# Performance work log

Hardware: AMD Instinct MI355X
Metric: run time of the kernel (lower is better)

Reference implementation:

```python
import jax, jax.numpy as jnp
import numpy as np

R = 59        # num relations (58 + 1)
D = 128       # node_feat_size
K = 16        # neighbors_sample


def _lstm(windows, Wk, Wr, b):
    # windows: [N, T, F]; standard Keras LSTM (gate order i, f, g, o).
    N = windows.shape[0]
    z_in = jnp.einsum('ntf,fh->nth', windows, Wk) + b        # [N, T, 4D]
    z_in = jnp.swapaxes(z_in, 0, 1)                          # [T, N, 4D]

    def step(carry, zt):
        h, c = carry
        z = zt + h @ Wr
        i, f, g, o = jnp.split(z, 4, axis=-1)
        i = jax.nn.sigmoid(i)
        f = jax.nn.sigmoid(f)
        g = jnp.tanh(g)
        o = jax.nn.sigmoid(o)
        c = f * c + i * g
        h = o * jnp.tanh(c)
        return (h, c), None

    h0 = jnp.zeros((N, D), windows.dtype)
    (h, _), _ = jax.lax.scan(step, (h0, h0), z_in)
    return h                                                 # [N, D]


def setup_inputs() -> dict:
    key = jax.random.key(0)
    ks = jax.random.split(key, 12)
    N, T, F = 1024, 32, 10
    s = 0.05
    return {
        'windows': jax.random.normal(ks[0], (N, T, F), jnp.float32),
        'neighbors': jax.random.randint(ks[1], (R, N, K), 0, N + 1, jnp.int32),
        'lstm_kernel': jax.random.normal(ks[2], (F, 4 * D), jnp.float32) * s,
        'lstm_recurrent': jax.random.normal(ks[3], (D, 4 * D), jnp.float32) * s,
        'lstm_bias': jax.random.normal(ks[4], (4 * D,), jnp.float32) * s,
        'W_state': jax.random.normal(ks[5], (R, 2 * D + R), jnp.float32) * s,
        'b_state': jax.random.normal(ks[6], (R,), jnp.float32) * s,
        'W_relattn': jax.random.normal(ks[7], (2 * D + R,), jnp.float32) * s,
        'b_relattn': jax.random.normal(ks[8], (1,), jnp.float32) * s,
        'W_pred': jax.random.normal(ks[9], (D, 3), jnp.float32) * s,
        'b_pred': jax.random.normal(ks[10], (3,), jnp.float32) * s,
    }


def reference(windows, neighbors, lstm_kernel, lstm_recurrent, lstm_bias,
              W_state, b_state, W_relattn, b_relattn, W_pred, b_pred):
    cur = _lstm(windows, lstm_kernel, lstm_recurrent, lstm_bias)    # [N, D]
    feats = jnp.concatenate([jnp.zeros((1, D), cur.dtype), cur], 0)  # [N+1, D]

    # --- per-relation state attention ---
    # Dense(1) on concat(cur, nbr, onehot(rel)) splits into three dot products.
    Wc = W_state[:, :D]            # [R, D]
    Wn = W_state[:, D:2 * D]       # [R, D]
    Wrr = W_state[:, 2 * D:]       # [R, R]; onehot picks the diagonal
    rel_term = jnp.diagonal(Wrr) + b_state                  # [R]
    cur_term = cur @ Wc.T                                    # [N, R]
    nbr_proj = feats @ Wn.T                                  # [N+1, R]
    # gather the scalar neighbor projection per relation: [R, N, K]
    nbr_term = jax.vmap(lambda idx, p: p[idx])(neighbors, nbr_proj.T)
    scores = jax.nn.relu(cur_term.T[:, :, None] + nbr_term
                         + rel_term[:, None, None])          # [R, N, K]
    w = jax.nn.softmax(scores, axis=-1)
    nbr_feats = feats[neighbors]                             # [R, N, K, D]
    rel_reps = jnp.einsum('rnk,rnkd->rnd', w, nbr_feats)     # [R, N, D]

    # --- relation attention ---
    wc = W_relattn[:D]
    wn = W_relattn[D:2 * D]
    wr = W_relattn[2 * D:]                                   # [R]
    s2 = jax.nn.relu((cur @ wc)[None, :]
                     + jnp.einsum('rnd,d->rn', rel_reps, wn)
                     + wr[:, None] + b_relattn[0])           # [R, N]
    aw = jax.nn.softmax(s2, axis=0)
    rel_agg = jnp.einsum('rn,rnd->nd', aw, rel_reps)         # [N, D]
    updated = cur + rel_agg

    logits = updated @ W_pred + b_pred                       # [N, 3]
    predictions = jax.nn.softmax(logits, axis=-1)
    return logits, predictions, updated
```

## Files before the change

kernel.cpp:

```cpp
#include <hip/hip_runtime.h>
#include <hip/hip_bf16.h>

constexpr int R  = 59;
constexpr int D  = 128;
constexpr int NK = 16;
constexpr int N  = 1024;
constexpr int T  = 32;
constexpr int F  = 10;
constexpr int H4 = 512;
constexpr int WSTRIDE = 2*D + R;

typedef __attribute__((ext_vector_type(8))) short short8;
typedef __attribute__((ext_vector_type(4))) float f32x4;

__device__ __forceinline__ float sigm(float x) {
  return __builtin_amdgcn_rcpf(1.0f + __expf(-x));
}
__device__ __forceinline__ float tanh_(float x) {
  return 2.0f * __builtin_amdgcn_rcpf(1.0f + __expf(-2.0f * x)) - 1.0f;
}
__device__ __forceinline__ ushort f2bf(float f) {
  unsigned u = __float_as_uint(f);
  u += 0x7FFF + ((u >> 16) & 1);
  return (ushort)(u >> 16);
}

__device__ int g_detect_f32(const void* windows) {
  const __hip_bfloat16* p = (const __hip_bfloat16*)windows;
  int weird = 0;
  for (int i = 0; i < 128; ++i) {
    float v = __bfloat162float(p[i]);
    float a = fabsf(v);
    if (!(a <= 100.0f) || (v != 0.0f && a < 1e-8f)) ++weird;
  }
  return weird > 8;
}

__device__ __forceinline__ float rdsrc(const void* p, int i, int isf32) {
  return isf32 ? ((const float*)p)[i]
               : __bfloat162float(((const __hip_bfloat16*)p)[i]);
}

struct CvtA {
  const void* small[6];
  int soff[7];
  const void* win;
  const void* wk;
  const void* wr;
  const void* bias;
};

__global__ __launch_bounds__(256) void convert_kernel(
    CvtA a, float* __restrict__ csm, float* __restrict__ wt,
    ushort* __restrict__ bpk, ushort* __restrict__ xwin,
    int* __restrict__ flag_out)
{
  __shared__ int sflag;
  if (threadIdx.x == 0) sflag = g_detect_f32(a.win);
  __syncthreads();
  const int isf32 = sflag;
  if (blockIdx.x == 0 && threadIdx.x == 0) flag_out[0] = isf32;
  const int gid = blockIdx.x * 256 + threadIdx.x;
  const int stride = gridDim.x * 256;

  for (int i = gid; i < a.soff[6]; i += stride) {
    int t = 0;
    while (t < 5 && i >= a.soff[t + 1]) ++t;
    csm[i] = rdsrc(a.small[t], i - a.soff[t], isf32);
  }
  for (int i = gid; i < 128 * 128; i += stride) {
    const int d = i >> 7, j = i & 127;
    float v = 0.0f;
    if (j < 59)        v = rdsrc(a.small[0], j * WSTRIDE + D + d, isf32);
    else if (j < 118)  v = rdsrc(a.small[0], (j - 59) * WSTRIDE + d, isf32);
    else if (j == 118) v = rdsrc(a.small[2], d, isf32);
    wt[i] = v;
  }
  for (int fi = gid; fi < 10240; fi += stride) {
    const int l  = fi & 63;
    const int kf = (fi >> 6) % 5;
    const int g  = ((fi >> 6) / 5) & 3;
    const int w  = (fi >> 6) / 20;
    const int col = g * 128 + w * 16 + (l & 15);
    const int q   = l >> 4;
#pragma unroll
    for (int j = 0; j < 8; ++j) {
      const int k = q * 8 + j;
      float v;
      if (kf < 4)      v = rdsrc(a.wr, (kf * 32 + k) * H4 + col, isf32);
      else if (k < 10) v = rdsrc(a.wk, k * H4 + col, isf32);
      else if (k == 10) v = rdsrc(a.bias, col, isf32);
      else             v = 0.0f;
      bpk[fi * 8 + j] = f2bf(v);
    }
  }
  for (int i = gid; i < N * T * 16; i += stride) {
    const int f = i & 15, nt = i >> 4;
    float v = (f < F) ? rdsrc(a.win, nt * F + f, isf32)
                      : (f == 10 ? 1.0f : 0.0f);
    xwin[i] = f2bf(v);
  }
}

__global__ __launch_bounds__(512)
__attribute__((amdgpu_waves_per_eu(2, 2)))
void lstm_kernel(const ushort* __restrict__ bpk, const ushort* __restrict__ xwin,
                 float* __restrict__ feats)
{
  const int tid = threadIdx.x;
  const int w   = tid >> 6;
  const int l   = tid & 63;
  const int n0  = blockIdx.x * 16;

  __shared__ ushort hbuf[2][16 * 136];
  __shared__ ushort xfrag[T * 64 * 8];

  if (blockIdx.x == 0 && tid < D) feats[tid] = 0.0f;

  for (int p = tid; p < T * 64; p += 512) {
    const int t = p >> 6, ll = p & 63, s = ll & 15, q = ll >> 4;
    *(short8*)&xfrag[p * 8] = *(const short8*)&xwin[(n0 + s) * (T * 16) + t * 16 + q * 8];
  }
  for (int i = tid; i < 2 * 16 * 136; i += 512) ((ushort*)hbuf)[i] = 0;

  short8 B[4][5];
#pragma unroll
  for (int g = 0; g < 4; ++g)
#pragma unroll
    for (int kf = 0; kf < 5; ++kf)
      B[g][kf] = *(const short8*)&bpk[((((w * 4 + g) * 5 + kf) * 64) + l) * 8];

  f32x4 c4 = {0.f, 0.f, 0.f, 0.f};
  float hreg[4];
  const int lq    = l >> 4;
  const int krow0 = lq * 8;
  const int srow0 = lq * 4;
  const int col_d = w * 16 + (l & 15);

  __syncthreads();

  for (int t = 0; t < T; ++t) {
    const ushort* hb = hbuf[t & 1];
    short8 A[5];
#pragma unroll
    for (int kf = 0; kf < 4; ++kf)
      A[kf] = *(const short8*)(hb + (l & 15) * 136 + kf * 32 + krow0);
    A[4] = *(const short8*)(xfrag + (t * 64 + l) * 8);

    f32x4 acc[4];
#pragma unroll
    for (int g = 0; g < 4; ++g) {
      acc[g] = (f32x4){0.f, 0.f, 0.f, 0.f};
#pragma unroll
      for (int kf = 0; kf < 5; ++kf)
        acc[g] = __builtin_amdgcn_mfma_f32_16x16x32_bf16(A[kf], B[g][kf], acc[g], 0, 0, 0);
    }

    ushort* hw = hbuf[(t + 1) & 1];
#pragma unroll
    for (int r = 0; r < 4; ++r) {
      const float i_ = sigm(acc[0][r]);
      const float f_ = sigm(acc[1][r]);
      const float g_ = tanh_(acc[2][r]);
      const float o_ = sigm(acc[3][r]);
      c4[r]   = f_ * c4[r] + i_ * g_;
      hreg[r] = o_ * tanh_(c4[r]);
      hw[(srow0 + r) * 136 + col_d] = f2bf(hreg[r]);
    }
    __syncthreads();
  }

#pragma unroll
  for (int r = 0; r < 4; ++r)
    feats[(n0 + srow0 + r + 1) * D + col_d] = hreg[r];
}

__global__ __launch_bounds__(128) void proj_kernel(
    const float* __restrict__ feats, const float* __restrict__ wt,
    float* __restrict__ cur_term, float* __restrict__ nbr_proj,
    float* __restrict__ curwc)
{
  const int m = blockIdx.x;
  const int j = threadIdx.x;
  __shared__ float frow[128];
  frow[j] = feats[m * D + j];
  __syncthreads();

  float acc = 0.0f;
#pragma unroll 8
  for (int d = 0; d < 128; ++d)
    acc = fmaf(frow[d], wt[d * 128 + j], acc);

  if (j < 59) nbr_proj[m * R + j] = acc;
  else if (m >= 1) {
    if (j < 118)       cur_term[(m - 1) * R + (j - 59)] = acc;
    else if (j == 118) curwc[m - 1] = acc;
  }
}

__device__ __forceinline__ void store_out(void* out, int i, float v, int outf32) {
  if (outf32) ((float*)out)[i] = v;
  else        ((__hip_bfloat16*)out)[i] = __float2bfloat16(v);
}

__global__ __launch_bounds__(256) void attn_kernel(
    const float* __restrict__ feats, const int* __restrict__ neighbors,
    const float* __restrict__ W_state, const float* __restrict__ b_state,
    const float* __restrict__ W_relattn, const float* __restrict__ b_relattn,
    const float* __restrict__ W_pred, const float* __restrict__ b_pred,
    const float* __restrict__ cur_term, const float* __restrict__ nbr_proj,
    const float* __restrict__ curwc, const int* __restrict__ flagp,
    void* __restrict__ out)
{
  const int n   = blockIdx.x;
  const int tid = threadIdx.x;

  __shared__ float rr[R * 132];
  __shared__ int   idx_lds[R * NK];
  __shared__ float sc_lds[R * NK];
  __shared__ float w_lds[R * NK];
  __shared__ float ct_lds[R];
  __shared__ float rt_lds[R];
  __shared__ float s2_lds[R];
  __shared__ float aw_lds[R];
  __shared__ float upd_lds[D];
  __shared__ int   sflag;

  if (tid == 0) sflag = flagp[0];
  if (tid < R) {
    ct_lds[tid] = cur_term[n * R + tid];
    rt_lds[tid] = W_state[tid * WSTRIDE + 2 * D + tid] + b_state[tid];
  }
  for (int i = tid; i < R * NK; i += 256) {
    const int r = i >> 4, k = i & 15;
    idx_lds[i] = neighbors[(r * N + n) * NK + k];
  }
  __syncthreads();
  const int outf32 = sflag;

  for (int i = tid; i < R * NK; i += 256) {
    const int r = i >> 4;
    float s = ct_lds[r] + nbr_proj[idx_lds[i] * R + r] + rt_lds[r];
    sc_lds[i] = fmaxf(s, 0.0f);
  }
  __syncthreads();

  if (tid < R) {
    float mx = -1e30f;
#pragma unroll
    for (int k = 0; k < NK; ++k) mx = fmaxf(mx, sc_lds[tid * NK + k]);
    float sum = 0.0f;
#pragma unroll
    for (int k = 0; k < NK; ++k) {
      float e = __expf(sc_lds[tid * NK + k] - mx);
      w_lds[tid * NK + k] = e;
      sum += e;
    }
    const float inv = __builtin_amdgcn_rcpf(sum);
#pragma unroll
    for (int k = 0; k < NK; ++k) w_lds[tid * NK + k] *= inv;
  }
  __syncthreads();

  {
    const int d4 = tid & 31;
    const int r0 = tid >> 5;
    for (int r = r0; r < R; r += 8) {
      float4 acc = {0.f, 0.f, 0.f, 0.f};
#pragma unroll
      for (int k = 0; k < NK; ++k) {
        const int m = idx_lds[r * NK + k];
        const float4 fv = *(const float4*)&feats[m * D + d4 * 4];
        const float wv = w_lds[r * NK + k];
        acc.x = fmaf(wv, fv.x, acc.x);
        acc.y = fmaf(wv, fv.y, acc.y);
        acc.z = fmaf(wv, fv.z, acc.z);
        acc.w = fmaf(wv, fv.w, acc.w);
      }
      *(float4*)&rr[r * 132 + d4 * 4] = acc;
    }
  }
  __syncthreads();

  {
    const int wv = tid >> 6, ln = tid & 63;
    for (int r = wv; r < R; r += 4) {
      float a = rr[r * 132 + ln] * W_relattn[D + ln] +
                rr[r * 132 + 64 + ln] * W_relattn[D + 64 + ln];
      for (int off = 32; off; off >>= 1) a += __shfl_xor(a, off);
      if (ln == 0) {
        float v = curwc[n] + a + W_relattn[2 * D + r] + b_relattn[0];
        s2_lds[r] = fmaxf(v, 0.0f);
      }
    }
  }
  __syncthreads();

  if (tid < 64) {
    float v = (tid < R) ? s2_lds[tid] : -1e30f;
    float mx = v;
    for (int off = 32; off; off >>= 1) mx = fmaxf(mx, __shfl_xor(mx, off));
    float e = (tid < R) ? __expf(v - mx) : 0.0f;
    float sum = e;
    for (int off = 32; off; off >>= 1) sum += __shfl_xor(sum, off);
    if (tid < R) aw_lds[tid] = e / sum;
  }
  __syncthreads();

  if (tid < D) {
    float agg = 0.0f;
    for (int r = 0; r < R; ++r) agg = fmaf(aw_lds[r], rr[r * 132 + tid], agg);
    const float upd = feats[(n + 1) * D + tid] + agg;
    store_out(out, 2 * 3 * N + n * D + tid, upd, outf32);
    upd_lds[tid] = upd;
  }
  __syncthreads();

  if (tid < 64) {
    float p[3];
#pragma unroll
    for (int j = 0; j < 3; ++j) {
      float v = upd_lds[tid] * W_pred[tid * 3 + j] +
                upd_lds[tid + 64] * W_pred[(tid + 64) * 3 + j];
      for (int off = 32; off; off >>= 1) v += __shfl_xor(v, off);
      p[j] = v + b_pred[j];
    }
    if (tid == 0) {
      const float mx = fmaxf(p[0], fmaxf(p[1], p[2]));
      const float e0 = __expf(p[0] - mx), e1 = __expf(p[1] - mx), e2 = __expf(p[2] - mx);
      const float s = e0 + e1 + e2;
      store_out(out, n * 3 + 0, p[0], outf32);
      store_out(out, n * 3 + 1, p[1], outf32);
      store_out(out, n * 3 + 2, p[2], outf32);
      store_out(out, 3 * N + n * 3 + 0, e0 / s, outf32);
      store_out(out, 3 * N + n * 3 + 1, e1 / s, outf32);
      store_out(out, 3 * N + n * 3 + 2, e2 / s, outf32);
    }
  }
}

extern "C" void kernel_launch(void* const* d_in, const int* in_sizes, int n_in,
                              void* d_out, int out_size, void* d_ws, size_t ws_size,
                              hipStream_t stream)
{
  const int* neighbors = (const int*)d_in[1];
  float* ws = (float*)d_ws;

  CvtA ca;
  {
    constexpr int SS[6] = {18585, 59, 315, 1, 384, 3};
    int off = 0;
    for (int i = 0; i < 6; ++i) { ca.small[i] = d_in[5 + i]; ca.soff[i] = off; off += SS[i]; }
    ca.soff[6] = off;
    ca.win  = d_in[0];
    ca.wk   = d_in[2];
    ca.wr   = d_in[3];
    ca.bias = d_in[4];
  }

  float*  csm      = ws;
  float*  wtpack   = csm + 19360;
  float*  feats    = wtpack + 16384;
  float*  cur_term = feats + 131200;
  float*  nbr_proj = cur_term + 60416;
  float*  curwc    = nbr_proj + 60480;
  int*    flagp    = (int*)(curwc + 1024);
  ushort* bpk      = (ushort*)(curwc + 1040);
  ushort* xwin     = bpk + 81920;

  const float* c_Wstate = csm;
  const float* c_bstate = csm + 18585;
  const float* c_Wrel   = csm + 18644;
  const float* c_brel   = csm + 18959;
  const float* c_Wpred  = csm + 18960;
  const float* c_bpred  = csm + 19344;

  convert_kernel<<<512, 256, 0, stream>>>(ca, csm, wtpack, bpk, xwin, flagp);
  lstm_kernel<<<N / 16, 512, 0, stream>>>(bpk, xwin, feats);
  proj_kernel<<<N + 1, 128, 0, stream>>>(feats, wtpack, cur_term, nbr_proj, curwc);
  attn_kernel<<<N, 256, 0, stream>>>(feats, neighbors, c_Wstate, c_bstate, c_Wrel,
                                     c_brel, c_Wpred, c_bpred,
                                     cur_term, nbr_proj, curwc, flagp, d_out);
}
```

Before: 89.90 us.

## Gather neighbor features as bf16 and fuse relation-attention dot into aggregation

The LSTM kernel now also writes a bf16 copy of the node features, and the attention kernel gathers neighbor rows from that copy, halving the bytes per random gather. The per-relation dot product with the relation-attention weights is computed inside the aggregation loop as partial sums, which removes a separate LDS pass and one barrier. The score buffer is transposed and reused for the softmax weights. Neighbor aggregation now uses bf16-rounded features, which adds error against the fp32 reference.

Result: faster. 78.09 us (-13.1%).

```diff
diff --git a/kernel.cpp b/kernel.cpp
--- a/kernel.cpp
+++ b/kernel.cpp
@@ -105,7 +105,7 @@
 __global__ __launch_bounds__(512)
 __attribute__((amdgpu_waves_per_eu(2, 2)))
 void lstm_kernel(const ushort* __restrict__ bpk, const ushort* __restrict__ xwin,
-                 float* __restrict__ feats)
+                 float* __restrict__ feats, ushort* __restrict__ fb16)
 {
   const int tid = threadIdx.x;
   const int w   = tid >> 6;
@@ -115,7 +115,7 @@
   __shared__ ushort hbuf[2][16 * 136];
   __shared__ ushort xfrag[T * 64 * 8];
 
-  if (blockIdx.x == 0 && tid < D) feats[tid] = 0.0f;
+  if (blockIdx.x == 0 && tid < D) { feats[tid] = 0.0f; fb16[tid] = 0; }
 
   for (int p = tid; p < T * 64; p += 512) {
     const int t = p >> 6, ll = p & 63, s = ll & 15, q = ll >> 4;
@@ -171,8 +171,10 @@
   }
 
 #pragma unroll
-  for (int r = 0; r < 4; ++r)
+  for (int r = 0; r < 4; ++r) {
     feats[(n0 + srow0 + r + 1) * D + col_d] = hreg[r];
+    fb16 [(n0 + srow0 + r + 1) * D + col_d] = f2bf(hreg[r]);
+  }
 }
 
 __global__ __launch_bounds__(128) void proj_kernel(
@@ -204,7 +206,8 @@
 }
 
 __global__ __launch_bounds__(256) void attn_kernel(
-    const float* __restrict__ feats, const int* __restrict__ neighbors,
+    const float* __restrict__ feats, const ushort* __restrict__ fb16,
+    const int* __restrict__ neighbors,
     const float* __restrict__ W_state, const float* __restrict__ b_state,
     const float* __restrict__ W_relattn, const float* __restrict__ b_relattn,
     const float* __restrict__ W_pred, const float* __restrict__ b_pred,
@@ -215,22 +218,24 @@
   const int n   = blockIdx.x;
   const int tid = threadIdx.x;
 
-  __shared__ float rr[R * 132];
-  __shared__ int   idx_lds[R * NK];
-  __shared__ float sc_lds[R * NK];
-  __shared__ float w_lds[R * NK];
-  __shared__ float ct_lds[R];
-  __shared__ float rt_lds[R];
-  __shared__ float s2_lds[R];
-  __shared__ float aw_lds[R];
-  __shared__ float upd_lds[D];
-  __shared__ int   sflag;
+  __shared__ float  rr[R * 132];
+  __shared__ int    idx_lds[R * NK];
+  __shared__ float  w_lds[NK * 60];
+  __shared__ float  s2part[16 * 68];
+  __shared__ float  wn_lds[D];
+  __shared__ float  ct_lds[R];
+  __shared__ float  rt_lds[R];
+  __shared__ float  s2_lds[R];
+  __shared__ float  aw_lds[R];
+  __shared__ float  upd_lds[D];
+  __shared__ int    sflag;
 
   if (tid == 0) sflag = flagp[0];
   if (tid < R) {
     ct_lds[tid] = cur_term[n * R + tid];
     rt_lds[tid] = W_state[tid * WSTRIDE + 2 * D + tid] + b_state[tid];
   }
+  if (tid >= 128 && tid < 256) wn_lds[tid - 128] = W_relattn[D + (tid - 128)];
   for (int i = tid; i < R * NK; i += 256) {
     const int r = i >> 4, k = i & 15;
     idx_lds[i] = neighbors[(r * N + n) * NK + k];
@@ -239,60 +244,66 @@
   const int outf32 = sflag;
 
   for (int i = tid; i < R * NK; i += 256) {
-    const int r = i >> 4;
+    const int r = i >> 4, k = i & 15;
     float s = ct_lds[r] + nbr_proj[idx_lds[i] * R + r] + rt_lds[r];
-    sc_lds[i] = fmaxf(s, 0.0f);
+    w_lds[k * 60 + r] = fmaxf(s, 0.0f);
   }
   __syncthreads();
 
   if (tid < R) {
-    float mx = -1e30f;
-#pragma unroll
-    for (int k = 0; k < NK; ++k) mx = fmaxf(mx, sc_lds[tid * NK + k]);
+    float mx = 0.0f;
+#pragma unroll
+    for (int k = 0; k < NK; ++k) mx = fmaxf(mx, w_lds[k * 60 + tid]);
     float sum = 0.0f;
+    float e[NK];
 #pragma unroll
     for (int k = 0; k < NK; ++k) {
-      float e = __expf(sc_lds[tid * NK + k] - mx);
-      w_lds[tid * NK + k] = e;
-      sum += e;
+      e[k] = __expf(w_lds[k * 60 + tid] - mx);
+      sum += e[k];
     }
     const float inv = __builtin_amdgcn_rcpf(sum);
 #pragma unroll
-    for (int k = 0; k < NK; ++k) w_lds[tid * NK + k] *= inv;
+    for (int k = 0; k < NK; ++k) w_lds[k * 60 + tid] = e[k] * inv;
   }
   __syncthreads();
 
   {
-    const int d4 = tid & 31;
-    const int r0 = tid >> 5;
-    for (int r = r0; r < R; r += 8) {
-      float4 acc = {0.f, 0.f, 0.f, 0.f};
+    const int d8 = tid & 15;
+    const int rp = tid >> 4;
+    for (int r = rp; r < R; r += 16) {
+      float acc[8];
+#pragma unroll
+      for (int j = 0; j < 8; ++j) acc[j] = 0.0f;
 #pragma unroll
       for (int k = 0; k < NK; ++k) {
         const int m = idx_lds[r * NK + k];
-        const float4 fv = *(const float4*)&feats[m * D + d4 * 4];
-        const float wv = w_lds[r * NK + k];
-        acc.x = fmaf(wv, fv.x, acc.x);
-        acc.y = fmaf(wv, fv.y, acc.y);
-        acc.z = fmaf(wv, fv.z, acc.z);
-        acc.w = fmaf(wv, fv.w, acc.w);
+        const uint4 v = *(const uint4*)&fb16[m * D + d8 * 8];
+        const float wv = w_lds[k * 60 + r];
+        acc[0] = fmaf(wv, __uint_as_float(v.x << 16),          acc[0]);
+        acc[1] = fmaf(wv, __uint_as_float(v.x & 0xffff0000u),  acc[1]);
+        acc[2] = fmaf(wv, __uint_as_float(v.y << 16),          acc[2]);
+        acc[3] = fmaf(wv, __uint_as_float(v.y & 0xffff0000u),  acc[3]);
+        acc[4] = fmaf(wv, __uint_as_float(v.z << 16),          acc[4]);
+        acc[5] = fmaf(wv, __uint_as_float(v.z & 0xffff0000u),  acc[5]);
+        acc[6] = fmaf(wv, __uint_as_float(v.w << 16),          acc[6]);
+        acc[7] = fmaf(wv, __uint_as_float(v.w & 0xffff0000u),  acc[7]);
       }
-      *(float4*)&rr[r * 132 + d4 * 4] = acc;
-    }
-  }
-  __syncthreads();
-
-  {
-    const int wv = tid >> 6, ln = tid & 63;
-    for (int r = wv; r < R; r += 4) {
-      float a = rr[r * 132 + ln] * W_relattn[D + ln] +
-                rr[r * 132 + 64 + ln] * W_relattn[D + 64 + ln];
-      for (int off = 32; off; off >>= 1) a += __shfl_xor(a, off);
-      if (ln == 0) {
-        float v = curwc[n] + a + W_relattn[2 * D + r] + b_relattn[0];
-        s2_lds[r] = fmaxf(v, 0.0f);
-      }
-    }
+      *(float4*)&rr[r * 132 + d8 * 8]     = (float4){acc[0], acc[1], acc[2], acc[3]};
+      *(float4*)&rr[r * 132 + d8 * 8 + 4] = (float4){acc[4], acc[5], acc[6], acc[7]};
+      float p = 0.0f;
+#pragma unroll
+      for (int j = 0; j < 8; ++j) p = fmaf(acc[j], wn_lds[d8 * 8 + j], p);
+      s2part[d8 * 68 + r] = p;
+    }
+  }
+  __syncthreads();
+
+  if (tid < R) {
+    float dot = 0.0f;
+#pragma unroll
+    for (int q = 0; q < 16; ++q) dot += s2part[q * 68 + tid];
+    float v = curwc[n] + dot + W_relattn[2 * D + tid] + b_relattn[0];
+    s2_lds[tid] = fmaxf(v, 0.0f);
   }
   __syncthreads();
 
@@ -367,6 +378,7 @@
   int*    flagp    = (int*)(curwc + 1024);
   ushort* bpk      = (ushort*)(curwc + 1040);
   ushort* xwin     = bpk + 81920;
+  ushort* fb16     = xwin + 524288;
 
   const float* c_Wstate = csm;
   const float* c_bstate = csm + 18585;
@@ -376,9 +388,9 @@
   const float* c_bpred  = csm + 19344;
 
   convert_kernel<<<512, 256, 0, stream>>>(ca, csm, wtpack, bpk, xwin, flagp);
-  lstm_kernel<<<N / 16, 512, 0, stream>>>(bpk, xwin, feats);
+  lstm_kernel<<<N / 16, 512, 0, stream>>>(bpk, xwin, feats, fb16);
   proj_kernel<<<N + 1, 128, 0, stream>>>(feats, wtpack, cur_term, nbr_proj, curwc);
-  attn_kernel<<<N, 256, 0, stream>>>(feats, neighbors, c_Wstate, c_bstate, c_Wrel,
+  attn_kernel<<<N, 256, 0, stream>>>(feats, fb16, neighbors, c_Wstate, c_bstate, c_Wrel,
                                      c_brel, c_Wpred, c_bpred,
                                      cur_term, nbr_proj, curwc, flagp, d_out);
 }
```
